# Kernel tuning notes

Hardware: AMD Instinct MI355X
Metric: run time of the kernel (lower is better)

The kernel has to match this reference:

```python
import jax, jax.numpy as jnp
import numpy as np

NS = 100000   # s-nodes (dtype==1, destinations)
NE = 100000   # e-nodes (dtype==2, sources)
EDG = 1600000 # edges e->s, avg degree 16
D = 256       # in_dim == out_dim
H = 8         # heads
HD = D // H   # head dim 32
FEAT = 64     # dst 'feat' size (hardcoded dstfeat_fc input)
DFF = 512     # ffn inner hidden


def setup_inputs() -> dict:
    key = jax.random.key(0)
    ks = jax.random.split(key, 12)
    s = jax.random.normal(ks[0], (NS, D), jnp.float32)
    e = jax.random.normal(ks[1], (NE, D), jnp.float32)
    dst_feat = jax.random.normal(ks[2], (NS, FEAT), jnp.float32)
    edge_src = jax.random.randint(ks[3], (EDG,), 0, NE)
    # guarantee every s-node has >=1 in-edge (first NS edges hit each dst once)
    rnd_dst = jax.random.randint(ks[4], (EDG,), 0, NS)
    edge_dst = jnp.where(jnp.arange(EDG) < NS, jnp.arange(EDG) % NS, rnd_dst)
    fc_w = jax.random.normal(ks[5], (H, D, HD), jnp.float32) / np.sqrt(D)
    dstfeat_w = jax.random.normal(ks[6], (H, FEAT, HD), jnp.float32) / np.sqrt(FEAT)
    proj_w = jax.random.normal(ks[7], (2 * D, D), jnp.float32) / np.sqrt(2 * D)
    proj_b = jnp.zeros((D,), jnp.float32)
    ln_g = jnp.ones((D,), jnp.float32)
    ln_b = jnp.zeros((D,), jnp.float32)
    w1 = jax.random.normal(ks[8], (D, DFF), jnp.float32) / np.sqrt(D)
    b1 = jnp.zeros((DFF,), jnp.float32)
    w2 = jax.random.normal(ks[9], (DFF, D), jnp.float32) / np.sqrt(DFF)
    b2 = jnp.zeros((D,), jnp.float32)
    return dict(s=s, e=e, dst_feat=dst_feat, fc_w=fc_w, dstfeat_w=dstfeat_w,
                proj_w=proj_w, proj_b=proj_b, ln_g=ln_g, ln_b=ln_b,
                w1=w1, b1=b1, w2=w2, b2=b2,
                edge_src=edge_src, edge_dst=edge_dst)


def _segment_softmax(scores, seg, n):
    # scores: [E, H], seg: [E] dst ids
    smax = jax.ops.segment_max(scores, seg, num_segments=n)  # [n, H], -inf for empty
    smax = jnp.where(jnp.isfinite(smax), smax, 0.0)
    ex = jnp.exp(scores - smax[seg])
    denom = jax.ops.segment_sum(ex, seg, num_segments=n)
    denom = jnp.where(denom > 0, denom, 1.0)
    return ex / denom[seg]


def reference(s, e, dst_feat, fc_w, dstfeat_w, proj_w, proj_b,
              ln_g, ln_b, w1, b1, w2, b2, edge_src, edge_dst):
    # per-head linear on source (e-node) features: [NE, H, HD]
    z = jnp.einsum('ni,hio->nho', e, fc_w)
    # per-head dst feature projection: [NS, H, HD]
    df = jnp.einsum('nf,hfo->nho', dst_feat, dstfeat_w)
    zs = z[edge_src]       # [E, H, HD] gather
    dfe = df[edge_dst]     # [E, H, HD]
    score = jnp.sum(zs * dfe, axis=-1)          # [E, H] per-edge dot score
    alpha = _segment_softmax(score, edge_dst, NS)
    hh = jax.ops.segment_sum(alpha[..., None] * zs, edge_dst, num_segments=NS)  # [NS, H, HD]
    h = hh.reshape(NS, H * HD)                  # concat heads
    h = jax.nn.elu(h)
    h = jnp.concatenate([h, s], axis=-1) @ proj_w + proj_b  # proj(cat(h, origin=s))
    # PositionwiseFeedForward (pre-LN, residual, gelu); dropout off (eval)
    mu = jnp.mean(h, axis=-1, keepdims=True)
    var = jnp.var(h, axis=-1, keepdims=True)
    xn = (h - mu) * jax.lax.rsqrt(var + 1e-6) * ln_g + ln_b
    out = h + (jax.nn.gelu(xn @ w1 + b1) @ w2 + b2)
    return out
```

## Files before the change

### kernel.cpp

```cpp
#include <hip/hip_runtime.h>
#include <hip/hip_bf16.h>
#include <stdint.h>

#define NS_N 100000
#define NE_N 100000
#define MP 100096
#define EDG_N 1600000
#define DIM 256
#define FEAT_N 64
#define DFF_N 512

using bf16 = __hip_bfloat16;
typedef __bf16 bf16x8 __attribute__((ext_vector_type(8)));
typedef float f32x4 __attribute__((ext_vector_type(4)));

__device__ __forceinline__ float toF(float x) { return x; }
__device__ __forceinline__ float toF(bf16 x) { return __bfloat162float(x); }

template <class T> __device__ __forceinline__ T fromF(float x);
template <> __device__ __forceinline__ float fromF<float>(float x) { return x; }
template <> __device__ __forceinline__ bf16 fromF<bf16>(float x) { return __float2bfloat16(x); }

__device__ __forceinline__ void g2l16(const void* g, void* l) {
    __builtin_amdgcn_global_load_lds((const __attribute__((address_space(1))) unsigned int*)g,
                                     (__attribute__((address_space(3))) unsigned int*)l, 16, 0, 0);
}

__global__ void cvt_f2b4(const float4* __restrict__ src, bf16* __restrict__ dst,
                         int M, int K4, int S) {
    int idx = blockIdx.x * 256 + threadIdx.x;
    if (idx >= M * K4) return;
    int r = idx / K4, c = (idx - r * K4) * 4;
    float4 v = src[idx];
    union { ushort4 u; bf16 h[4]; } p;
    p.h[0] = fromF<bf16>(v.x); p.h[1] = fromF<bf16>(v.y);
    p.h[2] = fromF<bf16>(v.z); p.h[3] = fromF<bf16>(v.w);
    *(ushort4*)&dst[(size_t)r * S + c] = p.u;
}

__global__ void tr_w(const float* __restrict__ src, bf16* __restrict__ dst, int K, int N) {
    int idx = blockIdx.x * 256 + threadIdx.x;
    if (idx >= K * N) return;
    int n = idx / K, k = idx - n * K;
    dst[idx] = fromF<bf16>(src[(size_t)k * N + n]);
}

__global__ void tr_headw(const float* __restrict__ src, bf16* __restrict__ dst, int K) {
    int idx = blockIdx.x * 256 + threadIdx.x;
    if (idx >= 256 * K) return;
    int n = idx / K, k = idx - n * K;
    dst[idx] = fromF<bf16>(src[((size_t)(n >> 5) * K + k) * 32 + (n & 31)]);
}

__global__ void count_edges(const int* __restrict__ edst, int* __restrict__ counts) {
    int t = blockIdx.x * 256 + threadIdx.x;
    if (t < EDG_N) atomicAdd(&counts[edst[t]], 1);
}

__global__ void scan_block(const int* __restrict__ counts, int* __restrict__ partial,
                           int* __restrict__ chunk) {
    __shared__ int sh[512];
    int i = blockIdx.x * 512 + threadIdx.x;
    int v = (i < NS_N) ? counts[i] : 0;
    sh[threadIdx.x] = v;
    __syncthreads();
    for (int off = 1; off < 512; off <<= 1) {
        int x = (threadIdx.x >= off) ? sh[threadIdx.x - off] : 0;
        __syncthreads();
        sh[threadIdx.x] += x;
        __syncthreads();
    }
    if (i < NS_N) partial[i] = sh[threadIdx.x] - v;
    if (threadIdx.x == 511) chunk[blockIdx.x] = sh[511];
}

__global__ void scan_chunks(int* __restrict__ chunk, int nc) {
    __shared__ int sh[256];
    int t = threadIdx.x;
    int v = (t < nc) ? chunk[t] : 0;
    sh[t] = v;
    __syncthreads();
    for (int off = 1; off < 256; off <<= 1) {
        int x = (t >= off) ? sh[t - off] : 0;
        __syncthreads();
        sh[t] += x;
        __syncthreads();
    }
    if (t < nc) chunk[t] = sh[t] - v;
}

__global__ void add_offsets(int* __restrict__ rowst, const int* __restrict__ chunk,
                            int* __restrict__ cursor) {
    int i = blockIdx.x * 256 + threadIdx.x;
    if (i < NS_N) {
        int r = rowst[i] + chunk[i >> 9];
        rowst[i] = r;
        cursor[i] = r;
    }
}

__global__ void scatter_edges(const int* __restrict__ esrc, const int* __restrict__ edst,
                              int* __restrict__ cursor, int* __restrict__ csr) {
    int t = blockIdx.x * 256 + threadIdx.x;
    if (t < EDG_N) {
        int d = edst[t];
        int pos = atomicAdd(&cursor[d], 1);
        csr[pos] = esrc[t];
    }
}

template <int K, int N, class TC, bool BIAS, bool GELU, bool RES>
__global__ __launch_bounds__(256) void mfma_gemm2(
    const bf16* __restrict__ A, const bf16* __restrict__ BT,
    const float* __restrict__ bias, const float* __restrict__ res,
    TC* __restrict__ C, int M) {
    static_assert(K % 32 == 0 && N % 256 == 0, "shape");
    constexpr int KS = K / 32;
    constexpr int CHUNKS = K / 32;
    __shared__ bf16 As[64 * K];

    const int tid = threadIdx.x;
    const int wave = tid >> 6, lane = tid & 63;
    const int m0 = blockIdx.x * 64;

#pragma unroll
    for (int c = 0; c < CHUNKS; ++c) {
        int off = c * 1024 + lane * 16;
        int riw = off / (K * 2);
        int slot = (off % (K * 2)) / 16;
        int row = wave * 16 + riw;
        const bf16* g = A + (size_t)(m0 + row) * K + (slot ^ (row & 7)) * 8;
        g2l16(g, As + (size_t)wave * 16 * K + c * 512);
    }
    __syncthreads();

    const int fr = lane & 15, q = lane >> 4;
    const int f7 = fr & 7;
    const int q4 = q * 4;

    for (int nc = wave * 64; nc < N; nc += 256) {
        f32x4 acc[4][4];
#pragma unroll
        for (int jt = 0; jt < 4; jt++) {
            const int col = nc + jt * 16 + fr;
            const float bv = BIAS ? bias[col] : 0.f;
#pragma unroll
            for (int mt = 0; mt < 4; mt++) {
#pragma unroll
                for (int r = 0; r < 4; r++) {
                    float v = bv;
                    if (RES) v += res[(size_t)(m0 + mt * 16 + q4 + r) * N + col];
                    acc[mt][jt][r] = v;
                }
            }
        }

        bf16x8 bcur[4];
#pragma unroll
        for (int jt = 0; jt < 4; jt++)
            bcur[jt] = *(const bf16x8*)(BT + (size_t)(nc + jt * 16 + fr) * K + q * 8);
#pragma unroll
        for (int ks = 0; ks < KS; ++ks) {
            bf16x8 bnxt[4];
            if (ks + 1 < KS) {
#pragma unroll
                for (int jt = 0; jt < 4; jt++)
                    bnxt[jt] = *(const bf16x8*)(BT + (size_t)(nc + jt * 16 + fr) * K + (ks + 1) * 32 + q * 8);
            }
            const int slot = (ks * 4 + q) ^ f7;
            bf16x8 af[4];
#pragma unroll
            for (int mt = 0; mt < 4; mt++)
                af[mt] = *(const bf16x8*)(As + (size_t)(mt * 16 + fr) * K + slot * 8);
#pragma unroll
            for (int mt = 0; mt < 4; mt++)
#pragma unroll
                for (int jt = 0; jt < 4; jt++)
                    acc[mt][jt] = __builtin_amdgcn_mfma_f32_16x16x32_bf16(af[mt], bcur[jt], acc[mt][jt], 0, 0, 0);
            if (ks + 1 < KS) {
#pragma unroll
                for (int jt = 0; jt < 4; jt++) bcur[jt] = bnxt[jt];
            }
        }

#pragma unroll
        for (int jt = 0; jt < 4; jt++) {
            const int col = nc + jt * 16 + fr;
#pragma unroll
            for (int mt = 0; mt < 4; mt++) {
#pragma unroll
                for (int r = 0; r < 4; r++) {
                    const int row = m0 + mt * 16 + q4 + r;
                    if (row < M) {
                        float v = acc[mt][jt][r];
                        if (GELU) {
                            float x = v;
                            float u = 0.7978845608028654f * (x + 0.044715f * x * x * x);
                            float eu = __expf(-2.f * fabsf(u));
                            float th = (1.f - eu) / (1.f + eu);
                            th = (u >= 0.f) ? th : -th;
                            v = 0.5f * x * (1.f + th);
                        }
                        C[(size_t)row * N + col] = fromF<TC>(v);
                    }
                }
            }
        }
    }
}

__device__ __forceinline__ float4 ldz4(const bf16* __restrict__ p) {
    ushort4 u = *(const ushort4*)p;
    float4 f;
    f.x = toF(*(const bf16*)&u.x);
    f.y = toF(*(const bf16*)&u.y);
    f.z = toF(*(const bf16*)&u.z);
    f.w = toF(*(const bf16*)&u.w);
    return f;
}

__device__ __forceinline__ float dot4(float4 a, float4 b) {
    return fmaf(a.x, b.x, fmaf(a.y, b.y, fmaf(a.z, b.z, a.w * b.w)));
}

__device__ __forceinline__ float hred8(float p) {
    p += __shfl_xor(p, 1);
    p += __shfl_xor(p, 2);
    p += __shfl_xor(p, 4);
    return p;
}

__global__ __launch_bounds__(256) void attn_k(
    const bf16* __restrict__ z, const bf16* __restrict__ df,
    const int* __restrict__ rowst, const int* __restrict__ counts,
    const int* __restrict__ csr, bf16* __restrict__ he) {
    const int dst = blockIdx.x * 4 + (threadIdx.x >> 6);
    if (dst >= NS_N) return;
    const int lane = threadIdx.x & 63;
    const int c4 = lane * 4;

    float4 dfv = ldz4(&df[(size_t)dst * DIM + c4]);

    const int rs = rowst[dst], deg = counts[dst];
    float m = -1e30f, l = 0.f;
    float4 acc = {0.f, 0.f, 0.f, 0.f};

    for (int c0 = 0; c0 < deg; c0 += 64) {
        const int nc = min(64, deg - c0);
        int idx = (lane < nc) ? csr[rs + c0 + lane] : 0;
        int j = 0;
        for (; j + 4 <= nc; j += 4) {
            int s0 = __shfl(idx, j);
            int s1 = __shfl(idx, j + 1);
            int s2 = __shfl(idx, j + 2);
            int s3 = __shfl(idx, j + 3);
            float4 z0 = ldz4(&z[(size_t)s0 * DIM + c4]);
            float4 z1 = ldz4(&z[(size_t)s1 * DIM + c4]);
            float4 z2 = ldz4(&z[(size_t)s2 * DIM + c4]);
            float4 z3 = ldz4(&z[(size_t)s3 * DIM + c4]);
            float p0 = hred8(dot4(z0, dfv));
            float p1 = hred8(dot4(z1, dfv));
            float p2 = hred8(dot4(z2, dfv));
            float p3 = hred8(dot4(z3, dfv));
            float nm = fmaxf(m, fmaxf(fmaxf(p0, p1), fmaxf(p2, p3)));
            float e0 = __expf(m - nm);
            float w0 = __expf(p0 - nm);
            float w1 = __expf(p1 - nm);
            float w2 = __expf(p2 - nm);
            float w3 = __expf(p3 - nm);
            l = fmaf(l, e0, (w0 + w1) + (w2 + w3));
            acc.x = fmaf(acc.x, e0, fmaf(w0, z0.x, fmaf(w1, z1.x, fmaf(w2, z2.x, w3 * z3.x))));
            acc.y = fmaf(acc.y, e0, fmaf(w0, z0.y, fmaf(w1, z1.y, fmaf(w2, z2.y, w3 * z3.y))));
            acc.z = fmaf(acc.z, e0, fmaf(w0, z0.z, fmaf(w1, z1.z, fmaf(w2, z2.z, w3 * z3.z))));
            acc.w = fmaf(acc.w, e0, fmaf(w0, z0.w, fmaf(w1, z1.w, fmaf(w2, z2.w, w3 * z3.w))));
            m = nm;
        }
        for (; j < nc; ++j) {
            int s0 = __shfl(idx, j);
            float4 z0 = ldz4(&z[(size_t)s0 * DIM + c4]);
            float p0 = hred8(dot4(z0, dfv));
            float nm = fmaxf(m, p0);
            float e0 = __expf(m - nm);
            float w0 = __expf(p0 - nm);
            l = fmaf(l, e0, w0);
            acc.x = fmaf(acc.x, e0, w0 * z0.x);
            acc.y = fmaf(acc.y, e0, w0 * z0.y);
            acc.z = fmaf(acc.z, e0, w0 * z0.z);
            acc.w = fmaf(acc.w, e0, w0 * z0.w);
            m = nm;
        }
    }

    const float invl = 1.f / l;
    float hx = acc.x * invl, hy = acc.y * invl, hz = acc.z * invl, hw = acc.w * invl;
    hx = (hx > 0.f) ? hx : expm1f(hx);
    hy = (hy > 0.f) ? hy : expm1f(hy);
    hz = (hz > 0.f) ? hz : expm1f(hz);
    hw = (hw > 0.f) ? hw : expm1f(hw);
    union { ushort4 u; bf16 h[4]; } o;
    o.h[0] = fromF<bf16>(hx);
    o.h[1] = fromF<bf16>(hy);
    o.h[2] = fromF<bf16>(hz);
    o.h[3] = fromF<bf16>(hw);
    *(ushort4*)&he[(size_t)dst * 512 + c4] = o.u;
}

__global__ __launch_bounds__(256) void ln_k(const float* __restrict__ h1,
                                            const float* __restrict__ g,
                                            const float* __restrict__ b,
                                            bf16* __restrict__ xn) {
    int row = blockIdx.x, t = threadIdx.x;
    float x = h1[(size_t)row * DIM + t];
    float s1 = x, s2 = x * x;
#pragma unroll
    for (int off = 32; off > 0; off >>= 1) {
        s1 += __shfl_xor(s1, off, 64);
        s2 += __shfl_xor(s2, off, 64);
    }
    __shared__ float red[2][4];
    int w = t >> 6;
    if ((t & 63) == 0) {
        red[0][w] = s1;
        red[1][w] = s2;
    }
    __syncthreads();
    float t1 = red[0][0] + red[0][1] + red[0][2] + red[0][3];
    float t2 = red[1][0] + red[1][1] + red[1][2] + red[1][3];
    float mu = t1 * (1.f / DIM);
    float var = t2 * (1.f / DIM) - mu * mu;
    float v = (x - mu) * rsqrtf(var + 1e-6f) * g[t] + b[t];
    xn[(size_t)row * DIM + t] = fromF<bf16>(v);
}

extern "C" void kernel_launch(void* const* d_in, const int* in_sizes, int n_in,
                              void* d_out, int out_size, void* d_ws, size_t ws_size,
                              hipStream_t stream) {
    const float* s = (const float*)d_in[0];
    const float* e = (const float*)d_in[1];
    const float* dst_feat = (const float*)d_in[2];
    const float* fc_w = (const float*)d_in[3];
    const float* dstfeat_w = (const float*)d_in[4];
    const float* proj_w = (const float*)d_in[5];
    const float* proj_b = (const float*)d_in[6];
    const float* ln_g = (const float*)d_in[7];
    const float* ln_b = (const float*)d_in[8];
    const float* w1 = (const float*)d_in[9];
    const float* b1 = (const float*)d_in[10];
    const float* w2 = (const float*)d_in[11];
    const float* b2 = (const float*)d_in[12];
    const int* edge_src = (const int*)d_in[13];
    const int* edge_dst = (const int*)d_in[14];
    float* out = (float*)d_out;

    char* base = (char*)d_ws;
    size_t off = 0;
    auto alloc = [&](size_t bytes) -> char* {
        char* p = base + off;
        off = (off + bytes + 255) & ~(size_t)255;
        return p;
    };
    bf16* fcT = (bf16*)alloc((size_t)256 * 256 * 2);
    bf16* dfeatT = (bf16*)alloc((size_t)256 * 64 * 2);
    bf16* projT = (bf16*)alloc((size_t)256 * 512 * 2);
    bf16* w1T = (bf16*)alloc((size_t)512 * 256 * 2);
    bf16* w2T = (bf16*)alloc((size_t)256 * 512 * 2);
    int* counts = (int*)alloc((size_t)NS_N * 4);
    int* rowst = (int*)alloc((size_t)NS_N * 4);
    int* cursor = (int*)alloc((size_t)NS_N * 4);
    int* chunks = (int*)alloc(1024);
    int* csr = (int*)alloc((size_t)EDG_N * 4);
    bf16* eB = (bf16*)alloc((size_t)MP * DIM * 2);
    bf16* zB = (bf16*)alloc((size_t)MP * DIM * 2);
    bf16* dfB = (bf16*)alloc((size_t)MP * DIM * 2);
    bf16* dfeatB = (bf16*)alloc((size_t)MP * FEAT_N * 2);
    bf16* catB = (bf16*)alloc((size_t)MP * 512 * 2);
    float* h1F = (float*)alloc((size_t)MP * DIM * 4);
    bf16* xnB = eB;
    bf16* a1B = zB;

    hipMemsetAsync(counts, 0, (size_t)NS_N * 4, stream);
    tr_headw<<<(256 * 256 + 255) / 256, 256, 0, stream>>>(fc_w, fcT, 256);
    tr_headw<<<(256 * 64 + 255) / 256, 256, 0, stream>>>(dstfeat_w, dfeatT, 64);
    tr_w<<<(512 * 256 + 255) / 256, 256, 0, stream>>>(proj_w, projT, 512, 256);
    tr_w<<<(256 * 512 + 255) / 256, 256, 0, stream>>>(w1, w1T, 256, 512);
    tr_w<<<(512 * 256 + 255) / 256, 256, 0, stream>>>(w2, w2T, 512, 256);
    cvt_f2b4<<<(NE_N * 64 + 255) / 256, 256, 0, stream>>>((const float4*)e, eB, NE_N, 64, DIM);
    cvt_f2b4<<<(NS_N * 16 + 255) / 256, 256, 0, stream>>>((const float4*)dst_feat, dfeatB, NS_N, 16, FEAT_N);
    cvt_f2b4<<<(NS_N * 64 + 255) / 256, 256, 0, stream>>>((const float4*)s, catB + 256, NS_N, 64, 512);
    count_edges<<<(EDG_N + 255) / 256, 256, 0, stream>>>(edge_dst, counts);
    int nchunk = (NS_N + 511) / 512;
    scan_block<<<nchunk, 512, 0, stream>>>(counts, rowst, chunks);
    scan_chunks<<<1, 256, 0, stream>>>(chunks, nchunk);
    add_offsets<<<(NS_N + 255) / 256, 256, 0, stream>>>(rowst, chunks, cursor);
    scatter_edges<<<(EDG_N + 255) / 256, 256, 0, stream>>>(edge_src, edge_dst, cursor, csr);

    dim3 blk(256);
    const int gb = MP / 64;
    mfma_gemm2<256, 256, bf16, false, false, false><<<gb, blk, 0, stream>>>(
        eB, fcT, nullptr, nullptr, zB, NE_N);
    mfma_gemm2<64, 256, bf16, false, false, false><<<gb, blk, 0, stream>>>(
        dfeatB, dfeatT, nullptr, nullptr, dfB, NS_N);
    attn_k<<<(NS_N + 3) / 4, 256, 0, stream>>>(zB, dfB, rowst, counts, csr, catB);
    mfma_gemm2<512, 256, float, true, false, false><<<gb, blk, 0, stream>>>(
        catB, projT, proj_b, nullptr, h1F, NS_N);
    ln_k<<<NS_N, 256, 0, stream>>>(h1F, ln_g, ln_b, xnB);
    mfma_gemm2<256, 512, bf16, true, true, false><<<gb, blk, 0, stream>>>(
        xnB, w1T, b1, nullptr, a1B, NS_N);
    mfma_gemm2<512, 256, float, true, false, true><<<gb, blk, 0, stream>>>(
        a1B, w2T, b2, h1F, out, NS_N);
}
```

Baseline: 1.097 ms.

## Retile MFMA GEMM with smaller row blocks, swapped operands and vectorized epilogue

Replaces the GEMM kernel with a variant that takes a templated row-block size (32 rows for K=512 GEMMs) and has each wave compute a 32-column strip per 128-column pass instead of 64 columns. The MFMA operands are swapped so each lane holds four consecutive output columns, which allows float4/ushort4 stores and float4 bias and residual loads. Launch bounds now request 4 blocks per SM. The aims are a smaller LDS footprint and fewer registers for higher occupancy, plus coalesced epilogue traffic, at the cost of reloading B fragments more often per row.

```diff
diff --git a/kernel.cpp b/kernel.cpp
--- a/kernel.cpp
+++ b/kernel.cpp
@@ -109,28 +109,30 @@
     }
 }
 
-template <int K, int N, class TC, bool BIAS, bool GELU, bool RES>
-__global__ __launch_bounds__(256) void mfma_gemm2(
+template <int BR, int K, int N, class TC, bool BIAS, bool GELU, bool RES>
+__global__ __launch_bounds__(256, 4) void mfma_gemm3(
     const bf16* __restrict__ A, const bf16* __restrict__ BT,
     const float* __restrict__ bias, const float* __restrict__ res,
     TC* __restrict__ C, int M) {
-    static_assert(K % 32 == 0 && N % 256 == 0, "shape");
+    static_assert(K % 32 == 0 && N % 128 == 0 && (BR == 32 || BR == 64), "shape");
+    constexpr int MT = BR / 16;
     constexpr int KS = K / 32;
-    constexpr int CHUNKS = K / 32;
-    __shared__ bf16 As[64 * K];
+    constexpr int CHUNKS = BR * K * 2 / 4096;
+    constexpr int WROWS = BR / 4;
+    __shared__ bf16 As[BR * K];
 
     const int tid = threadIdx.x;
     const int wave = tid >> 6, lane = tid & 63;
-    const int m0 = blockIdx.x * 64;
+    const int m0 = blockIdx.x * BR;
 
 #pragma unroll
     for (int c = 0; c < CHUNKS; ++c) {
         int off = c * 1024 + lane * 16;
         int riw = off / (K * 2);
         int slot = (off % (K * 2)) / 16;
-        int row = wave * 16 + riw;
+        int row = wave * WROWS + riw;
         const bf16* g = A + (size_t)(m0 + row) * K + (slot ^ (row & 7)) * 8;
-        g2l16(g, As + (size_t)wave * 16 * K + c * 512);
+        g2l16(g, As + (size_t)wave * WROWS * K + c * 512);
     }
     __syncthreads();
 
@@ -138,70 +140,84 @@
     const int f7 = fr & 7;
     const int q4 = q * 4;
 
-    for (int nc = wave * 64; nc < N; nc += 256) {
-        f32x4 acc[4][4];
-#pragma unroll
-        for (int jt = 0; jt < 4; jt++) {
-            const int col = nc + jt * 16 + fr;
-            const float bv = BIAS ? bias[col] : 0.f;
-#pragma unroll
-            for (int mt = 0; mt < 4; mt++) {
-#pragma unroll
-                for (int r = 0; r < 4; r++) {
-                    float v = bv;
-                    if (RES) v += res[(size_t)(m0 + mt * 16 + q4 + r) * N + col];
-                    acc[mt][jt][r] = v;
-                }
+    for (int cb0 = 0; cb0 < N; cb0 += 128) {
+        const int cb = cb0 + wave * 32;
+        f32x4 acc[MT][2];
+        const f32x4 zero4 = {0.f, 0.f, 0.f, 0.f};
+#pragma unroll
+        for (int mt = 0; mt < MT; mt++) {
+            acc[mt][0] = zero4;
+            acc[mt][1] = zero4;
+        }
+
+        const bf16* bp0 = BT + (size_t)(cb + fr) * K;
+        const bf16* bp1 = BT + (size_t)(cb + 16 + fr) * K;
+        bf16x8 bcur[2];
+        bcur[0] = *(const bf16x8*)(bp0 + q * 8);
+        bcur[1] = *(const bf16x8*)(bp1 + q * 8);
+#pragma unroll
+        for (int ks = 0; ks < KS; ++ks) {
+            bf16x8 bnxt[2];
+            if (ks + 1 < KS) {
+                bnxt[0] = *(const bf16x8*)(bp0 + (ks + 1) * 32 + q * 8);
+                bnxt[1] = *(const bf16x8*)(bp1 + (ks + 1) * 32 + q * 8);
+            }
+            const int slot = (ks * 4 + q) ^ f7;
+            bf16x8 af[MT];
+#pragma unroll
+            for (int mt = 0; mt < MT; mt++)
+                af[mt] = *(const bf16x8*)(As + (size_t)(mt * 16 + fr) * K + slot * 8);
+#pragma unroll
+            for (int mt = 0; mt < MT; mt++) {
+                acc[mt][0] = __builtin_amdgcn_mfma_f32_16x16x32_bf16(bcur[0], af[mt], acc[mt][0], 0, 0, 0);
+                acc[mt][1] = __builtin_amdgcn_mfma_f32_16x16x32_bf16(bcur[1], af[mt], acc[mt][1], 0, 0, 0);
+            }
+            if (ks + 1 < KS) {
+                bcur[0] = bnxt[0];
+                bcur[1] = bnxt[1];
             }
         }
 
-        bf16x8 bcur[4];
-#pragma unroll
-        for (int jt = 0; jt < 4; jt++)
-            bcur[jt] = *(const bf16x8*)(BT + (size_t)(nc + jt * 16 + fr) * K + q * 8);
-#pragma unroll
-        for (int ks = 0; ks < KS; ++ks) {
-            bf16x8 bnxt[4];
-            if (ks + 1 < KS) {
-#pragma unroll
-                for (int jt = 0; jt < 4; jt++)
-                    bnxt[jt] = *(const bf16x8*)(BT + (size_t)(nc + jt * 16 + fr) * K + (ks + 1) * 32 + q * 8);
-            }
-            const int slot = (ks * 4 + q) ^ f7;
-            bf16x8 af[4];
-#pragma unroll
-            for (int mt = 0; mt < 4; mt++)
-                af[mt] = *(const bf16x8*)(As + (size_t)(mt * 16 + fr) * K + slot * 8);
-#pragma unroll
-            for (int mt = 0; mt < 4; mt++)
-#pragma unroll
-                for (int jt = 0; jt < 4; jt++)
-                    acc[mt][jt] = __builtin_amdgcn_mfma_f32_16x16x32_bf16(af[mt], bcur[jt], acc[mt][jt], 0, 0, 0);
-            if (ks + 1 < KS) {
-#pragma unroll
-                for (int jt = 0; jt < 4; jt++) bcur[jt] = bnxt[jt];
-            }
-        }
-
-#pragma unroll
-        for (int jt = 0; jt < 4; jt++) {
-            const int col = nc + jt * 16 + fr;
-#pragma unroll
-            for (int mt = 0; mt < 4; mt++) {
-#pragma unroll
-                for (int r = 0; r < 4; r++) {
-                    const int row = m0 + mt * 16 + q4 + r;
-                    if (row < M) {
-                        float v = acc[mt][jt][r];
-                        if (GELU) {
-                            float x = v;
+#pragma unroll
+        for (int jt = 0; jt < 2; jt++) {
+            const int col = cb + jt * 16 + q4;
+            float4 bv4 = {0.f, 0.f, 0.f, 0.f};
+            if (BIAS) bv4 = *(const float4*)&bias[col];
+#pragma unroll
+            for (int mt = 0; mt < MT; mt++) {
+                const int row = m0 + mt * 16 + fr;
+                if (row < M) {
+                    float v0 = acc[mt][jt][0] + bv4.x;
+                    float v1 = acc[mt][jt][1] + bv4.y;
+                    float v2 = acc[mt][jt][2] + bv4.z;
+                    float v3 = acc[mt][jt][3] + bv4.w;
+                    if (RES) {
+                        float4 r4 = *(const float4*)&res[(size_t)row * N + col];
+                        v0 += r4.x; v1 += r4.y; v2 += r4.z; v3 += r4.w;
+                    }
+                    if (GELU) {
+                        float vv[4] = {v0, v1, v2, v3};
+#pragma unroll
+                        for (int r = 0; r < 4; r++) {
+                            float x = vv[r];
                             float u = 0.7978845608028654f * (x + 0.044715f * x * x * x);
                             float eu = __expf(-2.f * fabsf(u));
                             float th = (1.f - eu) / (1.f + eu);
                             th = (u >= 0.f) ? th : -th;
-                            v = 0.5f * x * (1.f + th);
+                            vv[r] = 0.5f * x * (1.f + th);
                         }
-                        C[(size_t)row * N + col] = fromF<TC>(v);
+                        v0 = vv[0]; v1 = vv[1]; v2 = vv[2]; v3 = vv[3];
+                    }
+                    if constexpr (sizeof(TC) == 4) {
+                        float4 o = {v0, v1, v2, v3};
+                        *(float4*)&C[(size_t)row * N + col] = o;
+                    } else {
+                        union { ushort4 u; bf16 h[4]; } o;
+                        o.h[0] = fromF<bf16>(v0);
+                        o.h[1] = fromF<bf16>(v1);
+                        o.h[2] = fromF<bf16>(v2);
+                        o.h[3] = fromF<bf16>(v3);
+                        *(ushort4*)&C[(size_t)row * N + col] = o.u;
                     }
                 }
             }
@@ -395,17 +411,16 @@
     scatter_edges<<<(EDG_N + 255) / 256, 256, 0, stream>>>(edge_src, edge_dst, cursor, csr);
 
     dim3 blk(256);
-    const int gb = MP / 64;
-    mfma_gemm2<256, 256, bf16, false, false, false><<<gb, blk, 0, stream>>>(
+    mfma_gemm3<64, 256, 256, bf16, false, false, false><<<MP / 64, blk, 0, stream>>>(
         eB, fcT, nullptr, nullptr, zB, NE_N);
-    mfma_gemm2<64, 256, bf16, false, false, false><<<gb, blk, 0, stream>>>(
+    mfma_gemm3<64, 64, 256, bf16, false, false, false><<<MP / 64, blk, 0, stream>>>(
         dfeatB, dfeatT, nullptr, nullptr, dfB, NS_N);
     attn_k<<<(NS_N + 3) / 4, 256, 0, stream>>>(zB, dfB, rowst, counts, csr, catB);
-    mfma_gemm2<512, 256, float, true, false, false><<<gb, blk, 0, stream>>>(
+    mfma_gemm3<32, 512, 256, float, true, false, false><<<MP / 32, blk, 0, stream>>>(
         catB, projT, proj_b, nullptr, h1F, NS_N);
     ln_k<<<NS_N, 256, 0, stream>>>(h1F, ln_g, ln_b, xnB);
-    mfma_gemm2<256, 512, bf16, true, true, false><<<gb, blk, 0, stream>>>(
+    mfma_gemm3<64, 256, 512, bf16, true, true, false><<<MP / 64, blk, 0, stream>>>(
         xnB, w1T, b1, nullptr, a1B, NS_N);
-    mfma_gemm2<512, 256, float, true, false, true><<<gb, blk, 0, stream>>>(
+    mfma_gemm3<32, 512, 256, float, true, false, true><<<MP / 32, blk, 0, stream>>>(
         a1B, w2T, b2, h1F, out, NS_N);
 }
```

Result: slower. 1.281 ms (+16.8%).
